# Kernel optimization log

Hardware: AMD Instinct MI355X
Metric: run time of the kernel (lower is better)

Reference implementation:

```python
import jax, jax.numpy as jnp
import numpy as np

N, E = 100000, 800000   # nodes, edges
H, F = 12, 8            # heads, per-head features
D = H * F               # 96 = num_in_features
LRELU_SLOPE = 0.2
LN_EPS = 1e-6


def setup_inputs() -> dict:
    key = jax.random.key(0)
    k1, k2, k3, k4, k5, k6 = jax.random.split(key, 6)
    x = jax.random.normal(k1, (N, D), dtype=jnp.float32)
    edge_index = jax.random.randint(k2, (2, E), 0, N, dtype=jnp.int64)
    # linear_proj: Linear(D, H*F, bias=False); init std = (D*H*F)**-0.5
    w_proj = jax.random.normal(k3, (D, D), dtype=jnp.float32) * (D * H * F) ** -0.5
    score_src = jax.random.normal(k4, (1, H, F), dtype=jnp.float32) * (H * F) ** -0.5
    score_trg = jax.random.normal(k5, (1, H, F), dtype=jnp.float32) * (H * F) ** -0.5
    ln_weight = jnp.ones((D,), dtype=jnp.float32)
    return {"x": x, "edge_index": edge_index, "w_proj": w_proj,
            "score_src": score_src, "score_trg": score_trg, "ln_weight": ln_weight}


def reference(x, edge_index, w_proj, score_src, score_trg, ln_weight):
    # dropout layers are identity (inference mode)
    src = edge_index[0]
    trg = edge_index[1]
    proj = x.reshape(N, H, F)                        # view, no projection (as in source)
    s_src = jnp.sum(proj * score_src, axis=-1)       # [N, H]
    s_trg = jnp.sum(proj * score_trg, axis=-1)       # [N, H]
    # lift to edges + leaky relu
    scores = s_src[src] + s_trg[trg]                 # [E, H]
    scores = jnp.where(scores >= 0, scores, LRELU_SLOPE * scores)
    # neighborhood-aware (segment) softmax over target nodes
    scores = scores - jnp.max(scores)
    exp_scores = jnp.exp(scores)                     # [E, H]
    denom = jax.ops.segment_sum(exp_scores, trg, num_segments=N)  # [N, H]
    attn = exp_scores / (denom[trg] + 1e-16)         # [E, H]
    # weighted aggregation of lifted source features
    weighted = proj[src] * attn[:, :, None]          # [E, H, F]
    agg = jax.ops.segment_sum(weighted, trg, num_segments=N)      # [N, H, F]
    out = agg.reshape(N, H * F)
    # RMS-style LayerNorm (no mean subtraction, weight only)
    var = jnp.mean(jnp.square(out.astype(jnp.float32)), axis=-1, keepdims=True)
    out = ln_weight * (out * jax.lax.rsqrt(var + LN_EPS))
    out = out @ w_proj.T                             # linear_proj, no bias
    return x + out
```

## Files before the change

kernel.cpp:

```cpp
#include <hip/hip_runtime.h>
#include <math.h>

#define NN 100000
#define EE 800000
#define HH 12
#define FF 8
#define DD 96
#define NBLK_SCAN 98
#define WROW 104

typedef __bf16 bf16x8 __attribute__((ext_vector_type(8)));
typedef float  f32x4  __attribute__((ext_vector_type(4)));

static __device__ __forceinline__ unsigned short f2bf(float f) {
    unsigned u = __builtin_bit_cast(unsigned, f);
    u += 0x7fffu + ((u >> 16) & 1u);
    return (unsigned short)(u >> 16);
}

__global__ __launch_bounds__(256) void k_scores(
    const float* __restrict__ x, const float* __restrict__ wsrc,
    const float* __restrict__ wtrg, float* __restrict__ s_src,
    float* __restrict__ s_trg)
{
    int tid = blockIdx.x * 256 + threadIdx.x;
    if (tid >= NN * HH) return;
    int h = tid % HH;
    int n = tid / HH;
    const float4* xp = (const float4*)(x + (size_t)n * DD + h * FF);
    float4 a = xp[0], b = xp[1];
    const float4* s4 = (const float4*)(wsrc + h * FF);
    const float4* t4 = (const float4*)(wtrg + h * FF);
    float4 sa = s4[0], sb = s4[1];
    float4 ta = t4[0], tb = t4[1];
    s_src[tid] = a.x*sa.x + a.y*sa.y + a.z*sa.z + a.w*sa.w
               + b.x*sb.x + b.y*sb.y + b.z*sb.z + b.w*sb.w;
    s_trg[tid] = a.x*ta.x + a.y*ta.y + a.z*ta.z + a.w*ta.w
               + b.x*tb.x + b.y*tb.y + b.z*tb.z + b.w*tb.w;
}

__global__ __launch_bounds__(256) void k_zero(int* __restrict__ counts)
{
    int i = blockIdx.x * 256 + threadIdx.x;
    if (i < NN) counts[i] = 0;
}

__global__ __launch_bounds__(256) void k_hist(const int* __restrict__ ei,
                                              int* __restrict__ counts)
{
    int e = blockIdx.x * 256 + threadIdx.x;
    if (e >= EE) return;
    int t = ei[EE + e];
    atomicAdd(&counts[t], 1);
}

__global__ __launch_bounds__(256) void k_scan1(const int* __restrict__ counts,
                                               int* __restrict__ bsum)
{
    __shared__ int sd[256];
    int t = threadIdx.x;
    int base = blockIdx.x * 1024 + t * 4;
    int s = 0;
    #pragma unroll
    for (int j = 0; j < 4; ++j) {
        int i = base + j;
        s += (i < NN) ? counts[i] : 0;
    }
    sd[t] = s;
    __syncthreads();
    for (int off = 128; off > 0; off >>= 1) {
        if (t < off) sd[t] += sd[t + off];
        __syncthreads();
    }
    if (t == 0) bsum[blockIdx.x] = sd[0];
}

__global__ __launch_bounds__(128) void k_scan2(const int* __restrict__ bsum,
                                               int* __restrict__ boff)
{
    __shared__ int sd[128];
    int t = threadIdx.x;
    sd[t] = (t < NBLK_SCAN) ? bsum[t] : 0;
    __syncthreads();
    for (int off = 1; off < 128; off <<= 1) {
        int u = (t >= off) ? sd[t - off] : 0;
        __syncthreads();
        sd[t] += u;
        __syncthreads();
    }
    if (t < NBLK_SCAN) boff[t] = (t == 0) ? 0 : sd[t - 1];
}

__global__ __launch_bounds__(256) void k_scan3(const int* __restrict__ counts,
                                               const int* __restrict__ boff,
                                               int* __restrict__ offsets,
                                               int* __restrict__ cursor)
{
    __shared__ int sd[256];
    int t = threadIdx.x;
    int base = blockIdx.x * 1024 + t * 4;
    int c[4];
    int s = 0;
    #pragma unroll
    for (int j = 0; j < 4; ++j) {
        int i = base + j;
        c[j] = (i < NN) ? counts[i] : 0;
        s += c[j];
    }
    sd[t] = s;
    __syncthreads();
    for (int off = 1; off < 256; off <<= 1) {
        int u = (t >= off) ? sd[t - off] : 0;
        __syncthreads();
        sd[t] += u;
        __syncthreads();
    }
    int run = boff[blockIdx.x] + ((t == 0) ? 0 : sd[t - 1]);
    #pragma unroll
    for (int j = 0; j < 4; ++j) {
        int i = base + j;
        if (i < NN) { offsets[i] = run; cursor[i] = run; }
        run += c[j];
    }
}

__global__ __launch_bounds__(256) void k_scatter(const int* __restrict__ ei,
                                                 int* __restrict__ cursor,
                                                 int* __restrict__ esrc)
{
    int e = blockIdx.x * 256 + threadIdx.x;
    if (e >= EE) return;
    int s = ei[e];
    int t = ei[EE + e];
    int pos = atomicAdd(&cursor[t], 1);
    esrc[pos] = s;
}

__global__ __launch_bounds__(192) void k_agg(
    const float* __restrict__ x, const float* __restrict__ s_src,
    const float* __restrict__ s_trg, const int* __restrict__ offsets,
    const int* __restrict__ counts, const int* __restrict__ esrc,
    const float* __restrict__ lnw, float* __restrict__ y)
{
    __shared__ float nsq[16];
    int t  = threadIdx.x;
    int ln = t / HH;
    int h  = t % HH;
    int n  = blockIdx.x * 16 + ln;
    if (t < 16) nsq[t] = 0.f;
    __syncthreads();

    float yp[8];
    bool valid = (n < NN);
    if (valid) {
        float st  = s_trg[n * HH + h];
        int beg   = offsets[n];
        int cnt   = counts[n];
        float denom = 0.f;
        float4 aa = {0.f, 0.f, 0.f, 0.f};
        float4 ab = {0.f, 0.f, 0.f, 0.f};
        for (int k = 0; k < cnt; ++k) {
            int s = esrc[beg + k];
            float sc = s_src[s * HH + h] + st;
            sc = (sc >= 0.f) ? sc : 0.2f * sc;
            float ex = __expf(sc);
            denom += ex;
            const float4* xp = (const float4*)(x + (size_t)s * DD + h * FF);
            float4 a = xp[0], b = xp[1];
            aa.x += a.x * ex; aa.y += a.y * ex; aa.z += a.z * ex; aa.w += a.w * ex;
            ab.x += b.x * ex; ab.y += b.y * ex; ab.z += b.z * ex; ab.w += b.w * ex;
        }
        float inv = 1.f / (denom + 1e-16f);
        yp[0] = aa.x * inv; yp[1] = aa.y * inv; yp[2] = aa.z * inv; yp[3] = aa.w * inv;
        yp[4] = ab.x * inv; yp[5] = ab.y * inv; yp[6] = ab.z * inv; yp[7] = ab.w * inv;
        float ss = 0.f;
        #pragma unroll
        for (int j = 0; j < 8; ++j) ss += yp[j] * yp[j];
        atomicAdd(&nsq[ln], ss);
    }
    __syncthreads();
    if (valid) {
        float scale = rsqrtf(nsq[ln] * (1.f / 96.f) + 1e-6f);
        const float4* lw = (const float4*)(lnw + h * FF);
        float4 w1 = lw[0], w2 = lw[1];
        float4 o1, o2;
        o1.x = yp[0] * scale * w1.x; o1.y = yp[1] * scale * w1.y;
        o1.z = yp[2] * scale * w1.z; o1.w = yp[3] * scale * w1.w;
        o2.x = yp[4] * scale * w2.x; o2.y = yp[5] * scale * w2.y;
        o2.z = yp[6] * scale * w2.z; o2.w = yp[7] * scale * w2.w;
        float4* yo = (float4*)(y + (size_t)n * DD + h * FF);
        yo[0] = o1; yo[1] = o2;
    }
}

__global__ __launch_bounds__(256) void k_out(
    const float* __restrict__ x, const float* __restrict__ y,
    const float* __restrict__ w, float* __restrict__ out)
{
    __shared__ char lds_raw[(96 + 64) * WROW * 2];
    unsigned short* wl = (unsigned short*)lds_raw;
    unsigned short* yl = ((unsigned short*)lds_raw) + 96 * WROW;
    int t  = threadIdx.x;
    int wv = t >> 6;
    int l  = t & 63;
    int tile = blockIdx.x * 64;
    int nrem = NN - tile;

    #pragma unroll
    for (int i = 0; i < 9; ++i) {
        int lin = t * 4 + i * 1024;
        int r = lin / 96, c = lin - (lin / 96) * 96;
        float4 v = *(const float4*)(w + lin);
        unsigned short* p = wl + r * WROW + c;
        p[0] = f2bf(v.x); p[1] = f2bf(v.y); p[2] = f2bf(v.z); p[3] = f2bf(v.w);
    }
    #pragma unroll
    for (int i = 0; i < 6; ++i) {
        int lin = t * 4 + i * 1024;
        int r = lin / 96, c = lin - (lin / 96) * 96;
        if (r < nrem) {
            float4 v = *(const float4*)(y + (size_t)tile * DD + lin);
            unsigned short* p = yl + r * WROW + c;
            p[0] = f2bf(v.x); p[1] = f2bf(v.y); p[2] = f2bf(v.z); p[3] = f2bf(v.w);
        }
    }
    __syncthreads();

    f32x4 acc[6] = {};
    int arow   = wv * 16 + (l & 15);
    int kchunk = (l >> 4) * 8;
    #pragma unroll
    for (int s = 0; s < 3; ++s) {
        bf16x8 af = *(const bf16x8*)(yl + arow * WROW + s * 32 + kchunk);
        #pragma unroll
        for (int nt = 0; nt < 6; ++nt) {
            bf16x8 bfr = *(const bf16x8*)(wl + (nt * 16 + (l & 15)) * WROW + s * 32 + kchunk);
            acc[nt] = __builtin_amdgcn_mfma_f32_16x16x32_bf16(af, bfr, acc[nt], 0, 0, 0);
        }
    }
    __syncthreads();

    float* fb = (float*)lds_raw;
    #pragma unroll
    for (int nt = 0; nt < 6; ++nt) {
        #pragma unroll
        for (int r = 0; r < 4; ++r) {
            int row = wv * 16 + (l >> 4) * 4 + r;
            int col = nt * 16 + (l & 15);
            fb[row * 97 + col] = acc[nt][r];
        }
    }
    __syncthreads();

    #pragma unroll
    for (int i = 0; i < 6; ++i) {
        int lin = t * 4 + i * 1024;
        int r = lin / 96, c = lin - (lin / 96) * 96;
        if (r < nrem) {
            float4 xv = *(const float4*)(x + (size_t)tile * DD + lin);
            float4 o;
            o.x = xv.x + fb[r * 97 + c + 0];
            o.y = xv.y + fb[r * 97 + c + 1];
            o.z = xv.z + fb[r * 97 + c + 2];
            o.w = xv.w + fb[r * 97 + c + 3];
            *(float4*)(out + (size_t)tile * DD + lin) = o;
        }
    }
}

extern "C" void kernel_launch(void* const* d_in, const int* in_sizes, int n_in,
                              void* d_out, int out_size, void* d_ws, size_t ws_size,
                              hipStream_t stream)
{
    const float* x    = (const float*)d_in[0];
    const int*   ei   = (const int*)d_in[1];
    const float* wprj = (const float*)d_in[2];
    const float* wsrc = (const float*)d_in[3];
    const float* wtrg = (const float*)d_in[4];
    const float* lnw  = (const float*)d_in[5];
    float* out = (float*)d_out;

    float* s_src  = (float*)d_ws;
    float* s_trg  = s_src + NN * HH;
    int*   counts = (int*)(s_trg + NN * HH);
    int*   offs   = counts + NN;
    int*   cursor = offs + NN;
    int*   bsum   = cursor + NN;
    int*   boff   = bsum + 128;
    int*   esrc   = boff + 128;
    float* y      = (float*)(esrc + EE);

    k_scores<<<(NN * HH + 255) / 256, 256, 0, stream>>>(x, wsrc, wtrg, s_src, s_trg);
    k_zero<<<(NN + 255) / 256, 256, 0, stream>>>(counts);
    k_hist<<<(EE + 255) / 256, 256, 0, stream>>>(ei, counts);
    k_scan1<<<NBLK_SCAN, 256, 0, stream>>>(counts, bsum);
    k_scan2<<<1, 128, 0, stream>>>(bsum, boff);
    k_scan3<<<NBLK_SCAN, 256, 0, stream>>>(counts, boff, offs, cursor);
    k_scatter<<<(EE + 255) / 256, 256, 0, stream>>>(ei, cursor, esrc);
    k_agg<<<(NN + 15) / 16, 192, 0, stream>>>(x, s_src, s_trg, offs, counts, esrc, lnw, y);
    k_out<<<(NN + 63) / 64, 256, 0, stream>>>(x, y, wprj, out);
}
```

Before: 276.0 us.

## Fuse aggregation with output projection and collapse scan into fewer kernels

Merges the per-node attention aggregation and RMS norm with the bf16 MFMA output projection into one 768-thread kernel, so normalized rows are written straight to LDS as bf16 instead of going through a global y buffer. The zeroing kernel is folded into the score kernel. The three-stage prefix scan becomes a single kernel by also counting per-1024-node chunks with atomics during the histogram. The aggregation loop prefetches the next source index. This removes global traffic and several launches, but adds a second atomic per edge and the cost of larger blocks with heavier LDS use.

```diff
diff --git a/kernel.cpp b/kernel.cpp
--- a/kernel.cpp
+++ b/kernel.cpp
@@ -17,13 +17,19 @@
     u += 0x7fffu + ((u >> 16) & 1u);
     return (unsigned short)(u >> 16);
 }
+static __device__ __forceinline__ unsigned packbf(float a, float b) {
+    return (unsigned)f2bf(a) | ((unsigned)f2bf(b) << 16);
+}
 
 __global__ __launch_bounds__(256) void k_scores(
     const float* __restrict__ x, const float* __restrict__ wsrc,
     const float* __restrict__ wtrg, float* __restrict__ s_src,
-    float* __restrict__ s_trg)
+    float* __restrict__ s_trg, int* __restrict__ counts,
+    int* __restrict__ chunks)
 {
     int tid = blockIdx.x * 256 + threadIdx.x;
+    if (tid < NN) counts[tid] = 0;
+    if (tid < 128) chunks[tid] = 0;
     if (tid >= NN * HH) return;
     int h = tid % HH;
     int n = tid / HH;
@@ -39,65 +45,35 @@
                + b.x*tb.x + b.y*tb.y + b.z*tb.z + b.w*tb.w;
 }
 
-__global__ __launch_bounds__(256) void k_zero(int* __restrict__ counts)
-{
-    int i = blockIdx.x * 256 + threadIdx.x;
-    if (i < NN) counts[i] = 0;
-}
-
 __global__ __launch_bounds__(256) void k_hist(const int* __restrict__ ei,
-                                              int* __restrict__ counts)
+                                              int* __restrict__ counts,
+                                              int* __restrict__ chunks)
 {
     int e = blockIdx.x * 256 + threadIdx.x;
     if (e >= EE) return;
     int t = ei[EE + e];
     atomicAdd(&counts[t], 1);
-}
-
-__global__ __launch_bounds__(256) void k_scan1(const int* __restrict__ counts,
-                                               int* __restrict__ bsum)
-{
+    atomicAdd(&chunks[t >> 10], 1);
+}
+
+__global__ __launch_bounds__(256) void k_scan(const int* __restrict__ counts,
+                                              const int* __restrict__ chunks,
+                                              int* __restrict__ offsets,
+                                              int* __restrict__ cursor)
+{
+    __shared__ int sc[128];
     __shared__ int sd[256];
     int t = threadIdx.x;
-    int base = blockIdx.x * 1024 + t * 4;
-    int s = 0;
-    #pragma unroll
-    for (int j = 0; j < 4; ++j) {
-        int i = base + j;
-        s += (i < NN) ? counts[i] : 0;
-    }
-    sd[t] = s;
-    __syncthreads();
-    for (int off = 128; off > 0; off >>= 1) {
-        if (t < off) sd[t] += sd[t + off];
-        __syncthreads();
-    }
-    if (t == 0) bsum[blockIdx.x] = sd[0];
-}
-
-__global__ __launch_bounds__(128) void k_scan2(const int* __restrict__ bsum,
-                                               int* __restrict__ boff)
-{
-    __shared__ int sd[128];
-    int t = threadIdx.x;
-    sd[t] = (t < NBLK_SCAN) ? bsum[t] : 0;
+    if (t < 128) sc[t] = (t < NBLK_SCAN) ? chunks[t] : 0;
     __syncthreads();
     for (int off = 1; off < 128; off <<= 1) {
-        int u = (t >= off) ? sd[t - off] : 0;
-        __syncthreads();
-        sd[t] += u;
-        __syncthreads();
-    }
-    if (t < NBLK_SCAN) boff[t] = (t == 0) ? 0 : sd[t - 1];
-}
-
-__global__ __launch_bounds__(256) void k_scan3(const int* __restrict__ counts,
-                                               const int* __restrict__ boff,
-                                               int* __restrict__ offsets,
-                                               int* __restrict__ cursor)
-{
-    __shared__ int sd[256];
-    int t = threadIdx.x;
+        int u = (t < 128 && t >= off) ? sc[t - off] : 0;
+        __syncthreads();
+        if (t < 128) sc[t] += u;
+        __syncthreads();
+    }
+    int bof = (blockIdx.x == 0) ? 0 : sc[blockIdx.x - 1];
+
     int base = blockIdx.x * 1024 + t * 4;
     int c[4];
     int s = 0;
@@ -115,7 +91,7 @@
         sd[t] += u;
         __syncthreads();
     }
-    int run = boff[blockIdx.x] + ((t == 0) ? 0 : sd[t - 1]);
+    int run = bof + ((t == 0) ? 0 : sd[t - 1]);
     #pragma unroll
     for (int j = 0; j < 4; ++j) {
         int i = base + j;
@@ -136,125 +112,111 @@
     esrc[pos] = s;
 }
 
-__global__ __launch_bounds__(192) void k_agg(
+__global__ __launch_bounds__(768) void k_aggout(
     const float* __restrict__ x, const float* __restrict__ s_src,
     const float* __restrict__ s_trg, const int* __restrict__ offsets,
     const int* __restrict__ counts, const int* __restrict__ esrc,
-    const float* __restrict__ lnw, float* __restrict__ y)
-{
-    __shared__ float nsq[16];
-    int t  = threadIdx.x;
-    int ln = t / HH;
-    int h  = t % HH;
-    int n  = blockIdx.x * 16 + ln;
-    if (t < 16) nsq[t] = 0.f;
-    __syncthreads();
-
-    float yp[8];
-    bool valid = (n < NN);
-    if (valid) {
-        float st  = s_trg[n * HH + h];
-        int beg   = offsets[n];
-        int cnt   = counts[n];
+    const float* __restrict__ lnw, const float* __restrict__ w,
+    float* __restrict__ out)
+{
+    __shared__ char lds_raw[(96 + 64) * WROW * 2];
+    __shared__ float nsq[64];
+    unsigned short* wl = (unsigned short*)lds_raw;
+    unsigned short* yl = ((unsigned short*)lds_raw) + 96 * WROW;
+    int t    = threadIdx.x;
+    int tile = blockIdx.x * 64;
+    int nrem = NN - tile;
+
+    if (t < 64) nsq[t] = 0.f;
+    #pragma unroll
+    for (int i = 0; i < 3; ++i) {
+        int lin = t * 4 + i * 3072;
+        int r = lin / 96, c = lin - (lin / 96) * 96;
+        float4 v = *(const float4*)(w + lin);
+        unsigned* p = (unsigned*)(wl + r * WROW + c);
+        p[0] = packbf(v.x, v.y); p[1] = packbf(v.z, v.w);
+    }
+    __syncthreads();
+
+    {
+        int ln = t / HH;
+        int h  = t - ln * HH;
+        int n  = tile + ln;
+        bool valid = (n < NN);
+        float st = 0.f; int beg = 0, cnt = 0;
+        if (valid) {
+            st  = s_trg[n * HH + h];
+            beg = offsets[n];
+            cnt = counts[n];
+        }
         float denom = 0.f;
         float4 aa = {0.f, 0.f, 0.f, 0.f};
         float4 ab = {0.f, 0.f, 0.f, 0.f};
+        int s_cur = (cnt > 0) ? esrc[beg] : 0;
         for (int k = 0; k < cnt; ++k) {
-            int s = esrc[beg + k];
-            float sc = s_src[s * HH + h] + st;
+            int s_nxt = (k + 1 < cnt) ? esrc[beg + k + 1] : 0;
+            float sc = s_src[s_cur * HH + h] + st;
             sc = (sc >= 0.f) ? sc : 0.2f * sc;
             float ex = __expf(sc);
             denom += ex;
-            const float4* xp = (const float4*)(x + (size_t)s * DD + h * FF);
+            const float4* xp = (const float4*)(x + (size_t)s_cur * DD + h * FF);
             float4 a = xp[0], b = xp[1];
             aa.x += a.x * ex; aa.y += a.y * ex; aa.z += a.z * ex; aa.w += a.w * ex;
             ab.x += b.x * ex; ab.y += b.y * ex; ab.z += b.z * ex; ab.w += b.w * ex;
+            s_cur = s_nxt;
         }
         float inv = 1.f / (denom + 1e-16f);
+        float yp[8];
         yp[0] = aa.x * inv; yp[1] = aa.y * inv; yp[2] = aa.z * inv; yp[3] = aa.w * inv;
         yp[4] = ab.x * inv; yp[5] = ab.y * inv; yp[6] = ab.z * inv; yp[7] = ab.w * inv;
         float ss = 0.f;
         #pragma unroll
         for (int j = 0; j < 8; ++j) ss += yp[j] * yp[j];
         atomicAdd(&nsq[ln], ss);
-    }
-    __syncthreads();
-    if (valid) {
+        __syncthreads();
         float scale = rsqrtf(nsq[ln] * (1.f / 96.f) + 1e-6f);
         const float4* lw = (const float4*)(lnw + h * FF);
         float4 w1 = lw[0], w2 = lw[1];
-        float4 o1, o2;
-        o1.x = yp[0] * scale * w1.x; o1.y = yp[1] * scale * w1.y;
-        o1.z = yp[2] * scale * w1.z; o1.w = yp[3] * scale * w1.w;
-        o2.x = yp[4] * scale * w2.x; o2.y = yp[5] * scale * w2.y;
-        o2.z = yp[6] * scale * w2.z; o2.w = yp[7] * scale * w2.w;
-        float4* yo = (float4*)(y + (size_t)n * DD + h * FF);
-        yo[0] = o1; yo[1] = o2;
-    }
-}
-
-__global__ __launch_bounds__(256) void k_out(
-    const float* __restrict__ x, const float* __restrict__ y,
-    const float* __restrict__ w, float* __restrict__ out)
-{
-    __shared__ char lds_raw[(96 + 64) * WROW * 2];
-    unsigned short* wl = (unsigned short*)lds_raw;
-    unsigned short* yl = ((unsigned short*)lds_raw) + 96 * WROW;
-    int t  = threadIdx.x;
+        unsigned* yo = (unsigned*)(yl + ln * WROW + h * FF);
+        yo[0] = packbf(yp[0] * scale * w1.x, yp[1] * scale * w1.y);
+        yo[1] = packbf(yp[2] * scale * w1.z, yp[3] * scale * w1.w);
+        yo[2] = packbf(yp[4] * scale * w2.x, yp[5] * scale * w2.y);
+        yo[3] = packbf(yp[6] * scale * w2.z, yp[7] * scale * w2.w);
+    }
+    __syncthreads();
+
     int wv = t >> 6;
     int l  = t & 63;
-    int tile = blockIdx.x * 64;
-    int nrem = NN - tile;
-
-    #pragma unroll
-    for (int i = 0; i < 9; ++i) {
-        int lin = t * 4 + i * 1024;
-        int r = lin / 96, c = lin - (lin / 96) * 96;
-        float4 v = *(const float4*)(w + lin);
-        unsigned short* p = wl + r * WROW + c;
-        p[0] = f2bf(v.x); p[1] = f2bf(v.y); p[2] = f2bf(v.z); p[3] = f2bf(v.w);
-    }
-    #pragma unroll
-    for (int i = 0; i < 6; ++i) {
-        int lin = t * 4 + i * 1024;
-        int r = lin / 96, c = lin - (lin / 96) * 96;
-        if (r < nrem) {
-            float4 v = *(const float4*)(y + (size_t)tile * DD + lin);
-            unsigned short* p = yl + r * WROW + c;
-            p[0] = f2bf(v.x); p[1] = f2bf(v.y); p[2] = f2bf(v.z); p[3] = f2bf(v.w);
-        }
-    }
-    __syncthreads();
-
-    f32x4 acc[6] = {};
-    int arow   = wv * 16 + (l & 15);
+    int tt0 = wv * 2;
+    int rt  = tt0 / 6;
+    int ct0 = tt0 - rt * 6;
     int kchunk = (l >> 4) * 8;
+    int arow = rt * 16 + (l & 15);
+    f32x4 acc0 = {}, acc1 = {};
     #pragma unroll
     for (int s = 0; s < 3; ++s) {
         bf16x8 af = *(const bf16x8*)(yl + arow * WROW + s * 32 + kchunk);
-        #pragma unroll
-        for (int nt = 0; nt < 6; ++nt) {
-            bf16x8 bfr = *(const bf16x8*)(wl + (nt * 16 + (l & 15)) * WROW + s * 32 + kchunk);
-            acc[nt] = __builtin_amdgcn_mfma_f32_16x16x32_bf16(af, bfr, acc[nt], 0, 0, 0);
-        }
+        bf16x8 b0 = *(const bf16x8*)(wl + ((ct0 + 0) * 16 + (l & 15)) * WROW + s * 32 + kchunk);
+        bf16x8 b1 = *(const bf16x8*)(wl + ((ct0 + 1) * 16 + (l & 15)) * WROW + s * 32 + kchunk);
+        acc0 = __builtin_amdgcn_mfma_f32_16x16x32_bf16(af, b0, acc0, 0, 0, 0);
+        acc1 = __builtin_amdgcn_mfma_f32_16x16x32_bf16(af, b1, acc1, 0, 0, 0);
     }
     __syncthreads();
 
     float* fb = (float*)lds_raw;
-    #pragma unroll
-    for (int nt = 0; nt < 6; ++nt) {
+    {
+        int row = rt * 16 + (l >> 4) * 4;
+        int col = ct0 * 16 + (l & 15);
         #pragma unroll
         for (int r = 0; r < 4; ++r) {
-            int row = wv * 16 + (l >> 4) * 4 + r;
-            int col = nt * 16 + (l & 15);
-            fb[row * 97 + col] = acc[nt][r];
-        }
-    }
-    __syncthreads();
-
-    #pragma unroll
-    for (int i = 0; i < 6; ++i) {
-        int lin = t * 4 + i * 1024;
+            fb[(row + r) * 97 + col]      = acc0[r];
+            fb[(row + r) * 97 + col + 16] = acc1[r];
+        }
+    }
+    __syncthreads();
+    #pragma unroll
+    for (int i = 0; i < 2; ++i) {
+        int lin = t * 4 + i * 3072;
         int r = lin / 96, c = lin - (lin / 96) * 96;
         if (r < nrem) {
             float4 xv = *(const float4*)(x + (size_t)tile * DD + lin);
@@ -285,18 +247,12 @@
     int*   counts = (int*)(s_trg + NN * HH);
     int*   offs   = counts + NN;
     int*   cursor = offs + NN;
-    int*   bsum   = cursor + NN;
-    int*   boff   = bsum + 128;
-    int*   esrc   = boff + 128;
-    float* y      = (float*)(esrc + EE);
-
-    k_scores<<<(NN * HH + 255) / 256, 256, 0, stream>>>(x, wsrc, wtrg, s_src, s_trg);
-    k_zero<<<(NN + 255) / 256, 256, 0, stream>>>(counts);
-    k_hist<<<(EE + 255) / 256, 256, 0, stream>>>(ei, counts);
-    k_scan1<<<NBLK_SCAN, 256, 0, stream>>>(counts, bsum);
-    k_scan2<<<1, 128, 0, stream>>>(bsum, boff);
-    k_scan3<<<NBLK_SCAN, 256, 0, stream>>>(counts, boff, offs, cursor);
+    int*   chunks = cursor + NN;
+    int*   esrc   = chunks + 128;
+
+    k_scores<<<(NN * HH + 255) / 256, 256, 0, stream>>>(x, wsrc, wtrg, s_src, s_trg, counts, chunks);
+    k_hist<<<(EE + 255) / 256, 256, 0, stream>>>(ei, counts, chunks);
+    k_scan<<<NBLK_SCAN, 256, 0, stream>>>(counts, chunks, offs, cursor);
     k_scatter<<<(EE + 255) / 256, 256, 0, stream>>>(ei, cursor, esrc);
-    k_agg<<<(NN + 15) / 16, 192, 0, stream>>>(x, s_src, s_trg, offs, counts, esrc, lnw, y);
-    k_out<<<(NN + 63) / 64, 256, 0, stream>>>(x, y, wprj, out);
-}
+    k_aggout<<<(NN + 63) / 64, 768, 0, stream>>>(x, s_src, s_trg, offs, counts, esrc, lnw, wprj, out);
+}
```

Result: slower. 1.068 ms (+286.9%).
